# Optimization experiments

Hardware: AMD Instinct MI355X
Metric: run time of the kernel (lower is better)

The kernel has to match this reference:

```python
import jax, jax.numpy as jnp
import numpy as np

FEAT = 512
HEADS = 8
HEAD_DIM = FEAT // HEADS
HIDDEN = 2048
EPS = 1e-5


def _linear(x, W, b):
    # torch Linear: y = x @ W.T + b, W: (out, in)
    return jnp.einsum('bnd,od->bno', x, W) + b


def _layernorm(x, g, b):
    mu = jnp.mean(x, axis=-1, keepdims=True)
    var = jnp.var(x, axis=-1, keepdims=True)
    return (x - mu) * jax.lax.rsqrt(var + EPS) * g + b


def setup_inputs() -> dict:
    key = jax.random.key(0)
    ks = jax.random.split(key, 16)
    bsz, N = 16, 512
    gain = 2 ** (-0.5)
    lim = gain * np.sqrt(6.0 / (FEAT + FEAT))
    inp = {
        'nfeat': jax.random.normal(ks[0], (bsz, N, FEAT), jnp.float32),
        'attn_bias': jax.random.normal(ks[1], (bsz, N, N, HEADS), jnp.float32),
        'attn_mask': jax.random.randint(ks[2], (bsz, N, N), 0, 2, jnp.int32),
        'Wq': jax.random.uniform(ks[3], (FEAT, FEAT), jnp.float32, -lim, lim),
        'bq': jnp.zeros((FEAT,), jnp.float32),
        'Wk': jax.random.uniform(ks[4], (FEAT, FEAT), jnp.float32, -lim, lim),
        'bk': jnp.zeros((FEAT,), jnp.float32),
        'Wv': jax.random.uniform(ks[5], (FEAT, FEAT), jnp.float32, -lim, lim),
        'bv': jnp.zeros((FEAT,), jnp.float32),
        'Wo': jax.random.uniform(ks[6], (FEAT, FEAT), jnp.float32, -np.sqrt(6.0/(2*FEAT)), np.sqrt(6.0/(2*FEAT))),
        'bo': jnp.zeros((FEAT,), jnp.float32),
        'W1': jax.random.normal(ks[7], (HIDDEN, FEAT), jnp.float32) * 0.02,
        'b1': jnp.zeros((HIDDEN,), jnp.float32),
        'W2': jax.random.normal(ks[8], (FEAT, HIDDEN), jnp.float32) * 0.02,
        'b2': jnp.zeros((FEAT,), jnp.float32),
        'ln1_g': jnp.ones((FEAT,), jnp.float32),
        'ln1_b': jnp.zeros((FEAT,), jnp.float32),
        'ln2_g': jnp.ones((FEAT,), jnp.float32),
        'ln2_b': jnp.zeros((FEAT,), jnp.float32),
    }
    return inp


def reference(nfeat, attn_bias, attn_mask, Wq, bq, Wk, bk, Wv, bv, Wo, bo,
              W1, b1, W2, b2, ln1_g, ln1_b, ln2_g, ln2_b):
    bsz, N, _ = nfeat.shape
    residual = nfeat
    # --- biased multi-head attention (norm_first=False => no pre-norm) ---
    q = _linear(nfeat, Wq, bq).reshape(bsz, N, HEADS, HEAD_DIM)
    k = _linear(nfeat, Wk, bk).reshape(bsz, N, HEADS, HEAD_DIM)
    v = _linear(nfeat, Wv, bv).reshape(bsz, N, HEADS, HEAD_DIM)
    # NOTE: original code does q / scaling with scaling = head_dim**-0.5,
    # i.e. scores are MULTIPLIED by sqrt(head_dim) (faithful to source).
    scale = jnp.float32(HEAD_DIM ** 0.5)
    scores = jnp.einsum('bqhd,bkhd->bhqk', q, k) * scale  # (b,h,N,N)
    scores = scores + jnp.transpose(attn_bias, (0, 3, 1, 2))  # additive bias
    mask = (attn_mask != 0)[:, None, :, :]
    scores = jnp.where(mask, -jnp.inf, scores)
    attn = jax.nn.softmax(scores, axis=-1)
    ctx = jnp.einsum('bhqk,bkhd->bqhd', attn, v).reshape(bsz, N, FEAT)
    out = _linear(ctx, Wo, bo)
    x = residual + out
    x = _layernorm(x, ln1_g, ln1_b)
    # --- FFN ---
    residual = x
    h = jax.nn.relu(_linear(x, W1, b1))
    h = _linear(h, W2, b2)
    x = residual + h
    x = _layernorm(x, ln2_g, ln2_b)
    return x
```

## Files before the change

### kernel.cpp

```cpp
#include <hip/hip_runtime.h>
#include <hip/hip_bf16.h>
#include <stdint.h>

typedef unsigned short u16;
typedef __attribute__((ext_vector_type(8))) __bf16 bf16x8;
typedef __attribute__((ext_vector_type(4))) float f32x4;
typedef __attribute__((ext_vector_type(4))) unsigned short u16x4;

#define B_   16
#define N_   512
#define D_   512
#define H_   8
#define DH_  64
#define HID_ 2048
#define M_   8192

__device__ __forceinline__ u16 f2bf(float f) {
    unsigned u = __float_as_uint(f);
    u += 0x7fffu + ((u >> 16) & 1u);
    return (u16)(u >> 16);
}
__device__ __forceinline__ float bf2f(u16 u) {
    return __uint_as_float(((unsigned)u) << 16);
}
__device__ __forceinline__ f32x4 mfma16(bf16x8 a, bf16x8 b, f32x4 c) {
    return __builtin_amdgcn_mfma_f32_16x16x32_bf16(a, b, c, 0, 0, 0);
}
__device__ __forceinline__ void gload_lds16(const u16* g, u16* l) {
    __builtin_amdgcn_global_load_lds(
        (const __attribute__((address_space(1))) void*)g,
        (__attribute__((address_space(3))) void*)l, 16, 0, 0);
}

__device__ __forceinline__ void cvt4(const float* s, u16* d) {
    f32x4 v = *(const f32x4*)s;
    u16x4 o;
    o[0] = f2bf(v[0]); o[1] = f2bf(v[1]); o[2] = f2bf(v[2]); o[3] = f2bf(v[3]);
    *(u16x4*)d = o;
}
__device__ __forceinline__ void cvt4s(const float* s, u16* dh, u16* dl) {
    f32x4 v = *(const f32x4*)s;
    u16x4 oh, ol;
#pragma unroll
    for (int j = 0; j < 4; j++) {
        oh[j] = f2bf(v[j]);
        float r = v[j] - bf2f(oh[j]);
        ol[j] = f2bf(r);
    }
    *(u16x4*)dh = oh;
    *(u16x4*)dl = ol;
}

__global__ __launch_bounds__(256) void convert_all(
    const float* __restrict__ nf, const float* __restrict__ Wq,
    const float* __restrict__ Wk, const float* __restrict__ Wv,
    const float* __restrict__ Wo, const float* __restrict__ W1,
    const float* __restrict__ W2, const float* __restrict__ bq,
    const float* __restrict__ bk, const float* __restrict__ bv,
    u16* __restrict__ xh, u16* __restrict__ xl,
    u16* __restrict__ wqh, u16* __restrict__ wql,
    u16* __restrict__ wob, u16* __restrict__ w1b, u16* __restrict__ w2b,
    float* __restrict__ bqkv)
{
    long i = ((long)blockIdx.x * 256 + threadIdx.x) * 4;
    if (i < 4194304) { cvt4s(nf + i, xh + i, xl + i); return; }
    i -= 4194304;
    if (i < 786432) {
        const float* s = (i < 262144) ? (Wq + i)
                       : (i < 524288) ? (Wk + i - 262144) : (Wv + i - 524288);
        cvt4s(s, wqh + i, wql + i); return;
    }
    i -= 786432;
    if (i < 262144) { cvt4(Wo + i, wob + i); return; }
    i -= 262144;
    if (i < 1048576) { cvt4(W1 + i, w1b + i); return; }
    i -= 1048576;
    if (i < 1048576) { cvt4(W2 + i, w2b + i); return; }
    i -= 1048576;
    if (i < 1536) {
        const float* s = (i < 512) ? (bq + i) : (i < 1024 ? bk + i - 512 : bv + i - 1024);
        *(f32x4*)(bqkv + i) = *(const f32x4*)s;
    }
}

#define BM 128
#define BN 128
#define BK 32

__global__ __launch_bounds__(256) void gemm_qkv(
    const u16* __restrict__ Ah, const u16* __restrict__ Al,
    const u16* __restrict__ Wh, const u16* __restrict__ Wl,
    const float* __restrict__ bias,
    u16* __restrict__ Qh, u16* __restrict__ Ql,
    u16* __restrict__ Kh, u16* __restrict__ Kl, u16* __restrict__ Vt)
{
    __shared__ u16 sAh[BM * BK], sAl[BM * BK], sBh[BN * BK], sBl[BN * BK];
    const int Kdim = 512;
    const int tid = threadIdx.x;
    const int w = tid >> 6, lane = tid & 63;
    const int lr = lane & 15, lg = lane >> 4;
    const int nTn = 1536 / BN;
    const int tm = blockIdx.x / nTn, tn = blockIdx.x % nTn;
    const long m0 = (long)tm * BM, n0 = (long)tn * BN;
    const int which = (int)(n0 >> 9);
    const bool vpath = (which == 2);

    f32x4 acc[4][4];
#pragma unroll
    for (int i = 0; i < 4; i++)
#pragma unroll
        for (int j = 0; j < 4; j++) acc[i][j] = (f32x4){0.f, 0.f, 0.f, 0.f};

    const int e0 = w * 512 + lane * 8;
    const int r0 = e0 >> 5, c0 = e0 & 31;
    const int r1 = r0 + 64;
    const long gA0 = (long)r0 * Kdim + c0, gA1 = (long)r1 * Kdim + c0;
    const u16* pAh = Ah + m0 * Kdim;
    const u16* pAl = Al + m0 * Kdim;
    const u16* pBh = Wh + n0 * Kdim;
    const u16* pBl = Wl + n0 * Kdim;
    u16* dAh0 = sAh + w * 512; u16* dAh1 = sAh + w * 512 + 2048;
    u16* dAl0 = sAl + w * 512; u16* dAl1 = sAl + w * 512 + 2048;
    u16* dBh0 = sBh + w * 512; u16* dBh1 = sBh + w * 512 + 2048;
    u16* dBl0 = sBl + w * 512; u16* dBl1 = sBl + w * 512 + 2048;

    const int wr = (w >> 1) * 64, wc = (w & 1) * 64;

    for (int k0 = 0; k0 < Kdim; k0 += BK) {
        gload_lds16(pAh + gA0 + k0, dAh0);
        gload_lds16(pAh + gA1 + k0, dAh1);
        gload_lds16(pBh + gA0 + k0, dBh0);
        gload_lds16(pBh + gA1 + k0, dBh1);
        if (!vpath) {
            gload_lds16(pAl + gA0 + k0, dAl0);
            gload_lds16(pAl + gA1 + k0, dAl1);
            gload_lds16(pBl + gA0 + k0, dBl0);
            gload_lds16(pBl + gA1 + k0, dBl1);
        }
        __syncthreads();
        bf16x8 ah[4], bh[4];
#pragma unroll
        for (int i = 0; i < 4; i++) {
            int ra = (wr + i * 16 + lr) * BK + lg * 8;
            int rb = (wc + i * 16 + lr) * BK + lg * 8;
            ah[i] = *reinterpret_cast<const bf16x8*>(&sAh[ra]);
            bh[i] = *reinterpret_cast<const bf16x8*>(&sBh[rb]);
        }
        if (vpath) {
#pragma unroll
            for (int i = 0; i < 4; i++)
#pragma unroll
                for (int j = 0; j < 4; j++)
                    acc[i][j] = mfma16(ah[i], bh[j], acc[i][j]);
        } else {
            bf16x8 al[4], bl[4];
#pragma unroll
            for (int i = 0; i < 4; i++) {
                int ra = (wr + i * 16 + lr) * BK + lg * 8;
                int rb = (wc + i * 16 + lr) * BK + lg * 8;
                al[i] = *reinterpret_cast<const bf16x8*>(&sAl[ra]);
                bl[i] = *reinterpret_cast<const bf16x8*>(&sBl[rb]);
            }
#pragma unroll
            for (int i = 0; i < 4; i++)
#pragma unroll
                for (int j = 0; j < 4; j++) {
                    acc[i][j] = mfma16(ah[i], bh[j], acc[i][j]);
                    acc[i][j] = mfma16(ah[i], bl[j], acc[i][j]);
                    acc[i][j] = mfma16(al[i], bh[j], acc[i][j]);
                }
        }
        __syncthreads();
    }

#pragma unroll
    for (int i = 0; i < 4; i++) {
#pragma unroll
        for (int j = 0; j < 4; j++) {
#pragma unroll
            for (int r = 0; r < 4; r++) {
                long m = m0 + wr + i * 16 + lg * 4 + r;
                long n = n0 + wc + j * 16 + lr;
                float v = acc[i][j][r] + bias[n];
                int b = (int)(m >> 9), nn = (int)(m & 511);
                int h = ((int)n >> 6) & 7, dh = (int)n & 63;
                long bh_ = (long)b * 8 + h;
                if (which == 2) {
                    Vt[(bh_ * 64 + dh) * 512 + nn] = f2bf(v);
                } else {
                    u16 hi = f2bf(v);
                    u16 lo = f2bf(v - bf2f(hi));
                    long idx = (bh_ * 512 + nn) * 64 + dh;
                    if (which == 0) { Qh[idx] = hi; Ql[idx] = lo; }
                    else            { Kh[idx] = hi; Kl[idx] = lo; }
                }
            }
        }
    }
}

template<int EPI>
__global__ __launch_bounds__(256) void gemm_bt(
    const u16* __restrict__ A, const u16* __restrict__ W,
    const float* __restrict__ bias, const float* __restrict__ resid,
    float* __restrict__ outf, u16* __restrict__ outb,
    int Mdim, int Ndim, int Kdim)
{
    __shared__ u16 As[BM * BK];
    __shared__ u16 Bs[BN * BK];
    const int tid = threadIdx.x;
    const int w = tid >> 6, lane = tid & 63;
    const int lr = lane & 15, lg = lane >> 4;
    const int nTn = Ndim / BN;
    const int tm = blockIdx.x / nTn, tn = blockIdx.x % nTn;
    const long m0 = (long)tm * BM, n0 = (long)tn * BN;

    f32x4 acc[4][4];
#pragma unroll
    for (int i = 0; i < 4; i++)
#pragma unroll
        for (int j = 0; j < 4; j++) acc[i][j] = (f32x4){0.f, 0.f, 0.f, 0.f};

    const int e0 = w * 512 + lane * 8;
    const int r0 = e0 >> 5, c0 = e0 & 31;
    const int r1 = r0 + 64, c1 = c0;
    u16* As0 = As + w * 512;
    u16* As1 = As + w * 512 + 2048;
    u16* Bs0 = Bs + w * 512;
    u16* Bs1 = Bs + w * 512 + 2048;
    const u16* Ag = A + m0 * Kdim;
    const u16* Bg = W + n0 * Kdim;

    const int wr = (w >> 1) * 64, wc = (w & 1) * 64;

    for (int k0 = 0; k0 < Kdim; k0 += BK) {
        gload_lds16(Ag + (long)r0 * Kdim + k0 + c0, As0);
        gload_lds16(Ag + (long)r1 * Kdim + k0 + c1, As1);
        gload_lds16(Bg + (long)r0 * Kdim + k0 + c0, Bs0);
        gload_lds16(Bg + (long)r1 * Kdim + k0 + c1, Bs1);
        __syncthreads();
        bf16x8 af[4], bfr[4];
#pragma unroll
        for (int i = 0; i < 4; i++) {
            af[i]  = *reinterpret_cast<const bf16x8*>(&As[(wr + i * 16 + lr) * BK + lg * 8]);
            bfr[i] = *reinterpret_cast<const bf16x8*>(&Bs[(wc + i * 16 + lr) * BK + lg * 8]);
        }
#pragma unroll
        for (int i = 0; i < 4; i++)
#pragma unroll
            for (int j = 0; j < 4; j++)
                acc[i][j] = mfma16(af[i], bfr[j], acc[i][j]);
        __syncthreads();
    }

#pragma unroll
    for (int i = 0; i < 4; i++) {
#pragma unroll
        for (int j = 0; j < 4; j++) {
#pragma unroll
            for (int r = 0; r < 4; r++) {
                long m = m0 + wr + i * 16 + lg * 4 + r;
                long n = n0 + wc + j * 16 + lr;
                float v = acc[i][j][r];
                if (EPI == 1) {
                    long idx = m * Ndim + n;
                    outf[idx] = v + bias[n] + resid[idx];
                } else {
                    float t = v + bias[n];
                    t = t > 0.f ? t : 0.f;
                    outb[m * Ndim + n] = f2bf(t);
                }
            }
        }
    }
}

#define PLST 2116
#define PST  72

__global__ __launch_bounds__(512) void attn_kernel(
    const u16* __restrict__ Qh, const u16* __restrict__ Ql,
    const u16* __restrict__ Kh, const u16* __restrict__ Kl,
    const u16* __restrict__ Vt,
    const float* __restrict__ bias, const int* __restrict__ mask,
    u16* __restrict__ ctx)
{
    __shared__ float Bs[8 * PLST];
    __shared__ u16 Ps[8 * 32 * PST];
    const int tid = threadIdx.x;
    const int w = tid >> 6, lane = tid & 63;
    const int lr = lane & 15, lg = lane >> 4;
    const int b = blockIdx.x >> 4, qt = blockIdx.x & 15;
    const int bq0 = qt * 32;
    const long bh = (long)b * 8 + w;
    const u16* Qhp = Qh + bh * 512 * 64;
    const u16* Qlp = Ql + bh * 512 * 64;
    const u16* Khp = Kh + bh * 512 * 64;
    const u16* Klp = Kl + bh * 512 * 64;
    const u16* Vp  = Vt + bh * 64 * 512;

    const int sq = tid >> 4, st = tid & 15;
    const float* bias_row = bias + ((long)b * 512 + bq0 + sq) * 512 * 8;
    const int*   mask_row = mask + ((long)b * 512 + bq0 + sq) * 512;

    bf16x8 qhf[2][2], qlf[2][2];
#pragma unroll
    for (int mf = 0; mf < 2; mf++)
#pragma unroll
        for (int kk = 0; kk < 2; kk++) {
            long off = (long)(bq0 + mf * 16 + lr) * 64 + kk * 32 + lg * 8;
            qhf[mf][kk] = *reinterpret_cast<const bf16x8*>(&Qhp[off]);
            qlf[mf][kk] = *reinterpret_cast<const bf16x8*>(&Qlp[off]);
        }

    f32x4 of[2][4];
    float m_run[2][4], l_run[2][4];
#pragma unroll
    for (int mf = 0; mf < 2; mf++) {
#pragma unroll
        for (int df = 0; df < 4; df++) of[mf][df] = (f32x4){0.f, 0.f, 0.f, 0.f};
#pragma unroll
        for (int r = 0; r < 4; r++) { m_run[mf][r] = -1e30f; l_run[mf][r] = 0.f; }
    }

    float* Bw = Bs + w * PLST;
    u16* Pw = Ps + w * 32 * PST;

    for (int kt = 0; kt < 8; ++kt) {
        const int k0 = kt * 64;
        f32x4 breg[8];
        int mreg[8];
#pragma unroll
        for (int j = 0; j < 8; j++) {
            int f = st + j * 16;
            breg[j] = *(const f32x4*)(bias_row + (long)k0 * 8 + f * 4);
            mreg[j] = mask_row[k0 + (f >> 1)];
        }
        f32x4 s[2][4];
#pragma unroll
        for (int mf = 0; mf < 2; mf++)
#pragma unroll
            for (int kf = 0; kf < 4; kf++) s[mf][kf] = (f32x4){0.f, 0.f, 0.f, 0.f};
#pragma unroll
        for (int kf = 0; kf < 4; kf++) {
            long ko = (long)(k0 + kf * 16 + lr) * 64 + lg * 8;
            bf16x8 kh0 = *reinterpret_cast<const bf16x8*>(&Khp[ko]);
            bf16x8 kh1 = *reinterpret_cast<const bf16x8*>(&Khp[ko + 32]);
            bf16x8 kl0 = *reinterpret_cast<const bf16x8*>(&Klp[ko]);
            bf16x8 kl1 = *reinterpret_cast<const bf16x8*>(&Klp[ko + 32]);
#pragma unroll
            for (int mf = 0; mf < 2; mf++) {
                s[mf][kf] = mfma16(qhf[mf][0], kh0, s[mf][kf]);
                s[mf][kf] = mfma16(qhf[mf][1], kh1, s[mf][kf]);
                s[mf][kf] = mfma16(qhf[mf][0], kl0, s[mf][kf]);
                s[mf][kf] = mfma16(qhf[mf][1], kl1, s[mf][kf]);
                s[mf][kf] = mfma16(qlf[mf][0], kh0, s[mf][kf]);
                s[mf][kf] = mfma16(qlf[mf][1], kh1, s[mf][kf]);
            }
        }
        __syncthreads();
#pragma unroll
        for (int j = 0; j < 8; j++) {
            int f = st + j * 16;
            int k = f >> 1, h4 = (f & 1) * 4;
            bool msk = (mreg[j] != 0);
#pragma unroll
            for (int c = 0; c < 4; c++)
                Bs[(h4 + c) * PLST + sq * 66 + k] = msk ? -3e38f : breg[j][c];
        }
        __syncthreads();
#pragma unroll
        for (int mf = 0; mf < 2; mf++) {
#pragma unroll
            for (int r = 0; r < 4; r++) {
                int qrow = mf * 16 + lg * 4 + r;
#pragma unroll
                for (int kf = 0; kf < 4; kf++) {
                    int k = kf * 16 + lr;
                    s[mf][kf][r] = s[mf][kf][r] * 8.0f + Bw[qrow * 66 + k];
                }
            }
        }
#pragma unroll
        for (int mf = 0; mf < 2; mf++) {
#pragma unroll
            for (int r = 0; r < 4; r++) {
                float pm = s[mf][0][r];
#pragma unroll
                for (int kf = 1; kf < 4; kf++) pm = fmaxf(pm, s[mf][kf][r]);
                pm = fmaxf(pm, __shfl_xor(pm, 1));
                pm = fmaxf(pm, __shfl_xor(pm, 2));
                pm = fmaxf(pm, __shfl_xor(pm, 4));
                pm = fmaxf(pm, __shfl_xor(pm, 8));
                float mn = fmaxf(m_run[mf][r], pm);
                float fac = __expf(m_run[mf][r] - mn);
                m_run[mf][r] = mn;
                float rs = 0.f;
#pragma unroll
                for (int kf = 0; kf < 4; kf++) {
                    float p = __expf(s[mf][kf][r] - mn);
                    s[mf][kf][r] = p;
                    rs += p;
                }
                rs += __shfl_xor(rs, 1); rs += __shfl_xor(rs, 2);
                rs += __shfl_xor(rs, 4); rs += __shfl_xor(rs, 8);
                l_run[mf][r] = l_run[mf][r] * fac + rs;
#pragma unroll
                for (int df = 0; df < 4; df++) of[mf][df][r] *= fac;
            }
        }
#pragma unroll
        for (int mf = 0; mf < 2; mf++)
#pragma unroll
            for (int kf = 0; kf < 4; kf++)
#pragma unroll
                for (int r = 0; r < 4; r++)
                    Pw[(mf * 16 + lg * 4 + r) * PST + kf * 16 + lr] = f2bf(s[mf][kf][r]);
#pragma unroll
        for (int kk = 0; kk < 2; kk++) {
            bf16x8 pa[2];
#pragma unroll
            for (int mf = 0; mf < 2; mf++)
                pa[mf] = *reinterpret_cast<const bf16x8*>(
                    &Pw[(mf * 16 + lr) * PST + kk * 32 + lg * 8]);
#pragma unroll
            for (int df = 0; df < 4; df++) {
                bf16x8 vb = *reinterpret_cast<const bf16x8*>(
                    &Vp[(long)(df * 16 + lr) * 512 + k0 + kk * 32 + lg * 8]);
                of[0][df] = mfma16(pa[0], vb, of[0][df]);
                of[1][df] = mfma16(pa[1], vb, of[1][df]);
            }
        }
    }
#pragma unroll
    for (int mf = 0; mf < 2; mf++) {
#pragma unroll
        for (int r = 0; r < 4; r++) {
            int q = bq0 + mf * 16 + lg * 4 + r;
            float inv = 1.0f / l_run[mf][r];
            u16* crow = ctx + ((long)b * 512 + q) * 512 + w * 64;
#pragma unroll
            for (int df = 0; df < 4; df++)
                crow[df * 16 + lr] = f2bf(of[mf][df][r] * inv);
        }
    }
}

template<int WB>
__global__ __launch_bounds__(256) void ln_kernel(
    const float* __restrict__ xin, const float* __restrict__ g,
    const float* __restrict__ bta, float* __restrict__ fout, u16* __restrict__ bout)
{
    const int tid = threadIdx.x;
    const int w = tid >> 6, lane = tid & 63;
    const long row = (long)blockIdx.x * 4 + w;
    const float* xp = xin + row * 512 + lane * 8;
    f32x4 v0 = *(const f32x4*)(xp);
    f32x4 v1 = *(const f32x4*)(xp + 4);
    float sum = v0[0] + v0[1] + v0[2] + v0[3] + v1[0] + v1[1] + v1[2] + v1[3];
    float sq = v0[0]*v0[0] + v0[1]*v0[1] + v0[2]*v0[2] + v0[3]*v0[3]
             + v1[0]*v1[0] + v1[1]*v1[1] + v1[2]*v1[2] + v1[3]*v1[3];
#pragma unroll
    for (int m = 1; m <= 32; m <<= 1) {
        sum += __shfl_xor(sum, m);
        sq  += __shfl_xor(sq, m);
    }
    float mu = sum * (1.f / 512.f);
    float var = sq * (1.f / 512.f) - mu * mu;
    float rstd = rsqrtf(var + 1e-5f);
#pragma unroll
    for (int j = 0; j < 8; j++) {
        int c = lane * 8 + j;
        float x = (j < 4) ? v0[j] : v1[j - 4];
        float y = (x - mu) * rstd * g[c] + bta[c];
        fout[row * 512 + c] = y;
        if (WB) bout[row * 512 + c] = f2bf(y);
    }
}

extern "C" void kernel_launch(void* const* d_in, const int* in_sizes, int n_in,
                              void* d_out, int out_size, void* d_ws, size_t ws_size,
                              hipStream_t stream)
{
    const float* nfeat     = (const float*)d_in[0];
    const float* attn_bias = (const float*)d_in[1];
    const int*   attn_mask = (const int*)d_in[2];
    const float* Wq = (const float*)d_in[3];
    const float* bq = (const float*)d_in[4];
    const float* Wk = (const float*)d_in[5];
    const float* bk = (const float*)d_in[6];
    const float* Wv = (const float*)d_in[7];
    const float* bv = (const float*)d_in[8];
    const float* Wo = (const float*)d_in[9];
    const float* bo = (const float*)d_in[10];
    const float* W1 = (const float*)d_in[11];
    const float* b1 = (const float*)d_in[12];
    const float* W2 = (const float*)d_in[13];
    const float* b2 = (const float*)d_in[14];
    const float* ln1_g = (const float*)d_in[15];
    const float* ln1_b = (const float*)d_in[16];
    const float* ln2_g = (const float*)d_in[17];
    const float* ln2_b = (const float*)d_in[18];

    char* ws = (char*)d_ws;
    size_t off = 0;
    auto alloc = [&](size_t bytes) -> void* {
        void* p = ws + off;
        off += (bytes + 255) & ~(size_t)255;
        return p;
    };
    u16* xh    = (u16*)alloc((size_t)M_ * D_ * 2);
    u16* xl    = (u16*)alloc((size_t)M_ * D_ * 2);
    u16* wqh   = (u16*)alloc((size_t)1536 * 512 * 2);
    u16* wql   = (u16*)alloc((size_t)1536 * 512 * 2);
    u16* wob   = (u16*)alloc((size_t)512 * 512 * 2);
    u16* w1b   = (u16*)alloc((size_t)2048 * 512 * 2);
    u16* w2b   = (u16*)alloc((size_t)512 * 2048 * 2);
    float* bqkv = (float*)alloc(1536 * 4);
    u16* Qh    = (u16*)alloc((size_t)B_ * H_ * N_ * DH_ * 2);
    u16* Ql    = (u16*)alloc((size_t)B_ * H_ * N_ * DH_ * 2);
    u16* Kh    = (u16*)alloc((size_t)B_ * H_ * N_ * DH_ * 2);
    u16* Kl    = (u16*)alloc((size_t)B_ * H_ * N_ * DH_ * 2);
    u16* Vt    = (u16*)alloc((size_t)B_ * H_ * N_ * DH_ * 2);
    u16* ctx   = (u16*)alloc((size_t)M_ * D_ * 2);
    float* xres = (float*)alloc((size_t)M_ * D_ * 4);
    float* x1f  = (float*)alloc((size_t)M_ * D_ * 4);
    u16* x1b   = (u16*)alloc((size_t)M_ * D_ * 2);
    u16* hb    = (u16*)alloc((size_t)M_ * HID_ * 2);

    convert_all<<<7170, 256, 0, stream>>>(nfeat, Wq, Wk, Wv, Wo, W1, W2, bq, bk, bv,
                                          xh, xl, wqh, wql, wob, w1b, w2b, bqkv);
    gemm_qkv<<<(M_/BM) * (1536/BN), 256, 0, stream>>>(
        xh, xl, wqh, wql, bqkv, Qh, Ql, Kh, Kl, Vt);
    attn_kernel<<<B_ * 16, 512, 0, stream>>>(
        Qh, Ql, Kh, Kl, Vt, attn_bias, attn_mask, ctx);
    gemm_bt<1><<<(M_/BM) * (512/BN), 256, 0, stream>>>(
        ctx, wob, bo, nfeat, xres, nullptr, M_, 512, 512);
    ln_kernel<1><<<M_ / 4, 256, 0, stream>>>(xres, ln1_g, ln1_b, x1f, x1b);
    gemm_bt<2><<<(M_/BM) * (HID_/BN), 256, 0, stream>>>(
        x1b, w1b, b1, nullptr, nullptr, hb, M_, HID_, 512);
    gemm_bt<1><<<(M_/BM) * (512/BN), 256, 0, stream>>>(
        hb, w2b, b2, x1f, xres, nullptr, M_, 512, 2048);
    ln_kernel<0><<<M_ / 4, 256, 0, stream>>>(xres, ln2_g, ln2_b, (float*)d_out, nullptr);
}
```

Baseline: 516.5 us.

## Store Q/K/V in MFMA fragment layout and halve attention query tile with bias prefetch

The QKV GEMM epilogue now writes Q, K and V directly in a per-lane MFMA fragment order, so each attention lane reads its operand with one contiguous 16-byte load instead of strided row reads. The attention kernel drops from 32 to 16 query rows per block, doubling the grid to 512 blocks to raise occupancy and parallelism. It double-buffers the bias and mask register loads so the next tile's fetch is issued while the current tile computes, and it raises wave priority around the MFMA sequences. The cost is that K and V fragments are re-read twice as often across blocks, and the epilogue now writes scattered addresses.

```diff
diff --git a/kernel.cpp b/kernel.cpp
--- a/kernel.cpp
+++ b/kernel.cpp
@@ -14,6 +14,7 @@
 #define DH_  64
 #define HID_ 2048
 #define M_   8192
+#define FRAG_BH 32768
 
 __device__ __forceinline__ u16 f2bf(float f) {
     unsigned u = __float_as_uint(f);
@@ -91,8 +92,8 @@
     const u16* __restrict__ Ah, const u16* __restrict__ Al,
     const u16* __restrict__ Wh, const u16* __restrict__ Wl,
     const float* __restrict__ bias,
-    u16* __restrict__ Qh, u16* __restrict__ Ql,
-    u16* __restrict__ Kh, u16* __restrict__ Kl, u16* __restrict__ Vt)
+    u16* __restrict__ Qf, u16* __restrict__ Qlf,
+    u16* __restrict__ Kf, u16* __restrict__ Klf, u16* __restrict__ Vf)
 {
     __shared__ u16 sAh[BM * BK], sAl[BM * BK], sBh[BN * BK], sBl[BN * BK];
     const int Kdim = 512;
@@ -186,13 +187,18 @@
                 int h = ((int)n >> 6) & 7, dh = (int)n & 63;
                 long bh_ = (long)b * 8 + h;
                 if (which == 2) {
-                    Vt[(bh_ * 64 + dh) * 512 + nn] = f2bf(v);
+                    int df = dh >> 4, rho = dh & 15;
+                    int gam = (nn >> 3) & 3, e = nn & 7, nb32 = nn >> 5;
+                    Vf[bh_ * FRAG_BH + (((long)nb32 * 4 + df) * 64 + gam * 16 + rho) * 8 + e]
+                        = f2bf(v);
                 } else {
+                    int nb = nn >> 4, rho = nn & 15;
+                    int kk = dh >> 5, gam = (dh >> 3) & 3, e = dh & 7;
+                    long idx = bh_ * FRAG_BH + (((long)nb * 2 + kk) * 64 + gam * 16 + rho) * 8 + e;
                     u16 hi = f2bf(v);
                     u16 lo = f2bf(v - bf2f(hi));
-                    long idx = (bh_ * 512 + nn) * 64 + dh;
-                    if (which == 0) { Qh[idx] = hi; Ql[idx] = lo; }
-                    else            { Kh[idx] = hi; Kl[idx] = lo; }
+                    if (which == 0) { Qf[idx] = hi; Qlf[idx] = lo; }
+                    else            { Kf[idx] = hi; Klf[idx] = lo; }
                 }
             }
         }
@@ -275,174 +281,162 @@
     }
 }
 
-#define PLST 2116
+#define PLST 1060
 #define PST  72
 
 __global__ __launch_bounds__(512) void attn_kernel(
-    const u16* __restrict__ Qh, const u16* __restrict__ Ql,
-    const u16* __restrict__ Kh, const u16* __restrict__ Kl,
-    const u16* __restrict__ Vt,
+    const u16* __restrict__ Qf, const u16* __restrict__ Qlf,
+    const u16* __restrict__ Kf, const u16* __restrict__ Klf,
+    const u16* __restrict__ Vf,
     const float* __restrict__ bias, const int* __restrict__ mask,
     u16* __restrict__ ctx)
 {
     __shared__ float Bs[8 * PLST];
-    __shared__ u16 Ps[8 * 32 * PST];
+    __shared__ u16 Ps[8 * 16 * PST];
     const int tid = threadIdx.x;
     const int w = tid >> 6, lane = tid & 63;
     const int lr = lane & 15, lg = lane >> 4;
-    const int b = blockIdx.x >> 4, qt = blockIdx.x & 15;
-    const int bq0 = qt * 32;
+    const int b = blockIdx.x >> 5, qt = blockIdx.x & 31;
+    const int bq0 = qt * 16;
     const long bh = (long)b * 8 + w;
-    const u16* Qhp = Qh + bh * 512 * 64;
-    const u16* Qlp = Ql + bh * 512 * 64;
-    const u16* Khp = Kh + bh * 512 * 64;
-    const u16* Klp = Kl + bh * 512 * 64;
-    const u16* Vp  = Vt + bh * 64 * 512;
-
-    const int sq = tid >> 4, st = tid & 15;
+    const u16* Qfp  = Qf  + bh * FRAG_BH;
+    const u16* Qlfp = Qlf + bh * FRAG_BH;
+    const u16* Kfp  = Kf  + bh * FRAG_BH;
+    const u16* Klfp = Klf + bh * FRAG_BH;
+    const u16* Vfp  = Vf  + bh * FRAG_BH;
+
+    const int sq = tid >> 5, st = tid & 31;
     const float* bias_row = bias + ((long)b * 512 + bq0 + sq) * 512 * 8;
     const int*   mask_row = mask + ((long)b * 512 + bq0 + sq) * 512;
 
-    bf16x8 qhf[2][2], qlf[2][2];
-#pragma unroll
-    for (int mf = 0; mf < 2; mf++)
+    bf16x8 qhf[2], qlf[2];
+#pragma unroll
+    for (int kk = 0; kk < 2; kk++) {
+        long off = (((long)qt * 2 + kk) * 64 + lane) * 8;
+        qhf[kk] = *reinterpret_cast<const bf16x8*>(&Qfp[off]);
+        qlf[kk] = *reinterpret_cast<const bf16x8*>(&Qlfp[off]);
+    }
+
+    f32x4 of[4];
+    float m_run[4], l_run[4];
+#pragma unroll
+    for (int df = 0; df < 4; df++) of[df] = (f32x4){0.f, 0.f, 0.f, 0.f};
+#pragma unroll
+    for (int r = 0; r < 4; r++) { m_run[r] = -1e30f; l_run[r] = 0.f; }
+
+    float* Bw = Bs + w * PLST;
+    u16* Pw = Ps + w * 16 * PST;
+
+    f32x4 bA[4], bB[4];
+    int mA[4], mB[4];
+
+    auto loadbias = [&](int kt, f32x4 (&bb)[4], int (&mm)[4]) {
+#pragma unroll
+        for (int j = 0; j < 4; j++) {
+            int f = st + j * 32;
+            bb[j] = *(const f32x4*)(bias_row + (long)kt * 512 + f * 4);
+            mm[j] = mask_row[kt * 64 + (f >> 1)];
+        }
+    };
+
+    auto body = [&](int kt, f32x4 (&bc)[4], int (&mc)[4],
+                    f32x4 (&bn)[4], int (&mn)[4], bool pf) {
+        f32x4 s[4];
+#pragma unroll
+        for (int kf = 0; kf < 4; kf++) s[kf] = (f32x4){0.f, 0.f, 0.f, 0.f};
+#pragma unroll
+        for (int kf = 0; kf < 4; kf++) {
+            long kb = (((long)(kt * 4 + kf) * 2) * 64 + lane) * 8;
+            bf16x8 kh0 = *reinterpret_cast<const bf16x8*>(&Kfp[kb]);
+            bf16x8 kh1 = *reinterpret_cast<const bf16x8*>(&Kfp[kb + 512]);
+            bf16x8 kl0 = *reinterpret_cast<const bf16x8*>(&Klfp[kb]);
+            bf16x8 kl1 = *reinterpret_cast<const bf16x8*>(&Klfp[kb + 512]);
+            __builtin_amdgcn_s_setprio(1);
+            s[kf] = mfma16(qhf[0], kh0, s[kf]);
+            s[kf] = mfma16(qhf[1], kh1, s[kf]);
+            s[kf] = mfma16(qhf[0], kl0, s[kf]);
+            s[kf] = mfma16(qhf[1], kl1, s[kf]);
+            s[kf] = mfma16(qlf[0], kh0, s[kf]);
+            s[kf] = mfma16(qlf[1], kh1, s[kf]);
+            __builtin_amdgcn_s_setprio(0);
+        }
+        __syncthreads();
+#pragma unroll
+        for (int j = 0; j < 4; j++) {
+            int f = st + j * 32;
+            int k = f >> 1, h4 = (f & 1) * 4;
+            bool msk = (mc[j] != 0);
+#pragma unroll
+            for (int c = 0; c < 4; c++)
+                Bs[(h4 + c) * PLST + sq * 66 + k] = msk ? -3e38f : bc[j][c];
+        }
+        __syncthreads();
+        if (pf) loadbias(kt + 1, bn, mn);
+#pragma unroll
+        for (int r = 0; r < 4; r++) {
+            int qrow = lg * 4 + r;
+#pragma unroll
+            for (int kf = 0; kf < 4; kf++)
+                s[kf][r] = s[kf][r] * 8.0f + Bw[qrow * 66 + kf * 16 + lr];
+        }
+#pragma unroll
+        for (int r = 0; r < 4; r++) {
+            float pm = fmaxf(fmaxf(s[0][r], s[1][r]), fmaxf(s[2][r], s[3][r]));
+            pm = fmaxf(pm, __shfl_xor(pm, 1));
+            pm = fmaxf(pm, __shfl_xor(pm, 2));
+            pm = fmaxf(pm, __shfl_xor(pm, 4));
+            pm = fmaxf(pm, __shfl_xor(pm, 8));
+            float mn_ = fmaxf(m_run[r], pm);
+            float fac = __expf(m_run[r] - mn_);
+            m_run[r] = mn_;
+            float rs = 0.f;
+#pragma unroll
+            for (int kf = 0; kf < 4; kf++) {
+                float p = __expf(s[kf][r] - mn_);
+                s[kf][r] = p;
+                rs += p;
+            }
+            rs += __shfl_xor(rs, 1); rs += __shfl_xor(rs, 2);
+            rs += __shfl_xor(rs, 4); rs += __shfl_xor(rs, 8);
+            l_run[r] = l_run[r] * fac + rs;
+#pragma unroll
+            for (int df = 0; df < 4; df++) of[df][r] *= fac;
+        }
+#pragma unroll
+        for (int kf = 0; kf < 4; kf++)
+#pragma unroll
+            for (int r = 0; r < 4; r++)
+                Pw[(lg * 4 + r) * PST + kf * 16 + lr] = f2bf(s[kf][r]);
 #pragma unroll
         for (int kk = 0; kk < 2; kk++) {
-            long off = (long)(bq0 + mf * 16 + lr) * 64 + kk * 32 + lg * 8;
-            qhf[mf][kk] = *reinterpret_cast<const bf16x8*>(&Qhp[off]);
-            qlf[mf][kk] = *reinterpret_cast<const bf16x8*>(&Qlp[off]);
-        }
-
-    f32x4 of[2][4];
-    float m_run[2][4], l_run[2][4];
-#pragma unroll
-    for (int mf = 0; mf < 2; mf++) {
-#pragma unroll
-        for (int df = 0; df < 4; df++) of[mf][df] = (f32x4){0.f, 0.f, 0.f, 0.f};
-#pragma unroll
-        for (int r = 0; r < 4; r++) { m_run[mf][r] = -1e30f; l_run[mf][r] = 0.f; }
-    }
-
-    float* Bw = Bs + w * PLST;
-    u16* Pw = Ps + w * 32 * PST;
-
-    for (int kt = 0; kt < 8; ++kt) {
-        const int k0 = kt * 64;
-        f32x4 breg[8];
-        int mreg[8];
-#pragma unroll
-        for (int j = 0; j < 8; j++) {
-            int f = st + j * 16;
-            breg[j] = *(const f32x4*)(bias_row + (long)k0 * 8 + f * 4);
-            mreg[j] = mask_row[k0 + (f >> 1)];
-        }
-        f32x4 s[2][4];
-#pragma unroll
-        for (int mf = 0; mf < 2; mf++)
-#pragma unroll
-            for (int kf = 0; kf < 4; kf++) s[mf][kf] = (f32x4){0.f, 0.f, 0.f, 0.f};
-#pragma unroll
-        for (int kf = 0; kf < 4; kf++) {
-            long ko = (long)(k0 + kf * 16 + lr) * 64 + lg * 8;
-            bf16x8 kh0 = *reinterpret_cast<const bf16x8*>(&Khp[ko]);
-            bf16x8 kh1 = *reinterpret_cast<const bf16x8*>(&Khp[ko + 32]);
-            bf16x8 kl0 = *reinterpret_cast<const bf16x8*>(&Klp[ko]);
-            bf16x8 kl1 = *reinterpret_cast<const bf16x8*>(&Klp[ko + 32]);
-#pragma unroll
-            for (int mf = 0; mf < 2; mf++) {
-                s[mf][kf] = mfma16(qhf[mf][0], kh0, s[mf][kf]);
-                s[mf][kf] = mfma16(qhf[mf][1], kh1, s[mf][kf]);
-                s[mf][kf] = mfma16(qhf[mf][0], kl0, s[mf][kf]);
-                s[mf][kf] = mfma16(qhf[mf][1], kl1, s[mf][kf]);
-                s[mf][kf] = mfma16(qlf[mf][0], kh0, s[mf][kf]);
-                s[mf][kf] = mfma16(qlf[mf][1], kh1, s[mf][kf]);
-            }
-        }
-        __syncthreads();
-#pragma unroll
-        for (int j = 0; j < 8; j++) {
-            int f = st + j * 16;
-            int k = f >> 1, h4 = (f & 1) * 4;
-            bool msk = (mreg[j] != 0);
-#pragma unroll
-            for (int c = 0; c < 4; c++)
-                Bs[(h4 + c) * PLST + sq * 66 + k] = msk ? -3e38f : breg[j][c];
-        }
-        __syncthreads();
-#pragma unroll
-        for (int mf = 0; mf < 2; mf++) {
-#pragma unroll
-            for (int r = 0; r < 4; r++) {
-                int qrow = mf * 16 + lg * 4 + r;
-#pragma unroll
-                for (int kf = 0; kf < 4; kf++) {
-                    int k = kf * 16 + lr;
-                    s[mf][kf][r] = s[mf][kf][r] * 8.0f + Bw[qrow * 66 + k];
-                }
-            }
-        }
-#pragma unroll
-        for (int mf = 0; mf < 2; mf++) {
-#pragma unroll
-            for (int r = 0; r < 4; r++) {
-                float pm = s[mf][0][r];
-#pragma unroll
-                for (int kf = 1; kf < 4; kf++) pm = fmaxf(pm, s[mf][kf][r]);
-                pm = fmaxf(pm, __shfl_xor(pm, 1));
-                pm = fmaxf(pm, __shfl_xor(pm, 2));
-                pm = fmaxf(pm, __shfl_xor(pm, 4));
-                pm = fmaxf(pm, __shfl_xor(pm, 8));
-                float mn = fmaxf(m_run[mf][r], pm);
-                float fac = __expf(m_run[mf][r] - mn);
-                m_run[mf][r] = mn;
-                float rs = 0.f;
-#pragma unroll
-                for (int kf = 0; kf < 4; kf++) {
-                    float p = __expf(s[mf][kf][r] - mn);
-                    s[mf][kf][r] = p;
-                    rs += p;
-                }
-                rs += __shfl_xor(rs, 1); rs += __shfl_xor(rs, 2);
-                rs += __shfl_xor(rs, 4); rs += __shfl_xor(rs, 8);
-                l_run[mf][r] = l_run[mf][r] * fac + rs;
-#pragma unroll
-                for (int df = 0; df < 4; df++) of[mf][df][r] *= fac;
-            }
-        }
-#pragma unroll
-        for (int mf = 0; mf < 2; mf++)
-#pragma unroll
-            for (int kf = 0; kf < 4; kf++)
-#pragma unroll
-                for (int r = 0; r < 4; r++)
-                    Pw[(mf * 16 + lg * 4 + r) * PST + kf * 16 + lr] = f2bf(s[mf][kf][r]);
-#pragma unroll
-        for (int kk = 0; kk < 2; kk++) {
-            bf16x8 pa[2];
-#pragma unroll
-            for (int mf = 0; mf < 2; mf++)
-                pa[mf] = *reinterpret_cast<const bf16x8*>(
-                    &Pw[(mf * 16 + lr) * PST + kk * 32 + lg * 8]);
+            bf16x8 pa = *reinterpret_cast<const bf16x8*>(
+                &Pw[lr * PST + kk * 32 + lg * 8]);
 #pragma unroll
             for (int df = 0; df < 4; df++) {
                 bf16x8 vb = *reinterpret_cast<const bf16x8*>(
-                    &Vp[(long)(df * 16 + lr) * 512 + k0 + kk * 32 + lg * 8]);
-                of[0][df] = mfma16(pa[0], vb, of[0][df]);
-                of[1][df] = mfma16(pa[1], vb, of[1][df]);
+                    &Vfp[((((long)(kt * 2 + kk)) * 4 + df) * 64 + lane) * 8]);
+                __builtin_amdgcn_s_setprio(1);
+                of[df] = mfma16(pa, vb, of[df]);
+                __builtin_amdgcn_s_setprio(0);
             }
         }
-    }
-#pragma unroll
-    for (int mf = 0; mf < 2; mf++) {
-#pragma unroll
-        for (int r = 0; r < 4; r++) {
-            int q = bq0 + mf * 16 + lg * 4 + r;
-            float inv = 1.0f / l_run[mf][r];
-            u16* crow = ctx + ((long)b * 512 + q) * 512 + w * 64;
-#pragma unroll
-            for (int df = 0; df < 4; df++)
-                crow[df * 16 + lr] = f2bf(of[mf][df][r] * inv);
-        }
+    };
+
+    loadbias(0, bA, mA);
+#pragma unroll
+    for (int kt2 = 0; kt2 < 4; kt2++) {
+        body(kt2 * 2,     bA, mA, bB, mB, true);
+        body(kt2 * 2 + 1, bB, mB, bA, mA, kt2 < 3);
+    }
+
+#pragma unroll
+    for (int r = 0; r < 4; r++) {
+        int q = bq0 + lg * 4 + r;
+        float inv = 1.0f / l_run[r];
+        u16* crow = ctx + ((long)b * 512 + q) * 512 + w * 64;
+#pragma unroll
+        for (int df = 0; df < 4; df++)
+            crow[df * 16 + lr] = f2bf(of[df][r] * inv);
     }
 }
 
@@ -517,11 +511,11 @@
     u16* w1b   = (u16*)alloc((size_t)2048 * 512 * 2);
     u16* w2b   = (u16*)alloc((size_t)512 * 2048 * 2);
     float* bqkv = (float*)alloc(1536 * 4);
-    u16* Qh    = (u16*)alloc((size_t)B_ * H_ * N_ * DH_ * 2);
-    u16* Ql    = (u16*)alloc((size_t)B_ * H_ * N_ * DH_ * 2);
-    u16* Kh    = (u16*)alloc((size_t)B_ * H_ * N_ * DH_ * 2);
-    u16* Kl    = (u16*)alloc((size_t)B_ * H_ * N_ * DH_ * 2);
-    u16* Vt    = (u16*)alloc((size_t)B_ * H_ * N_ * DH_ * 2);
+    u16* Qf    = (u16*)alloc((size_t)128 * FRAG_BH * 2);
+    u16* Qlf   = (u16*)alloc((size_t)128 * FRAG_BH * 2);
+    u16* Kf    = (u16*)alloc((size_t)128 * FRAG_BH * 2);
+    u16* Klf   = (u16*)alloc((size_t)128 * FRAG_BH * 2);
+    u16* Vf    = (u16*)alloc((size_t)128 * FRAG_BH * 2);
     u16* ctx   = (u16*)alloc((size_t)M_ * D_ * 2);
     float* xres = (float*)alloc((size_t)M_ * D_ * 4);
     float* x1f  = (float*)alloc((size_t)M_ * D_ * 4);
@@ -531,9 +525,9 @@
     convert_all<<<7170, 256, 0, stream>>>(nfeat, Wq, Wk, Wv, Wo, W1, W2, bq, bk, bv,
                                           xh, xl, wqh, wql, wob, w1b, w2b, bqkv);
     gemm_qkv<<<(M_/BM) * (1536/BN), 256, 0, stream>>>(
-        xh, xl, wqh, wql, bqkv, Qh, Ql, Kh, Kl, Vt);
-    attn_kernel<<<B_ * 16, 512, 0, stream>>>(
-        Qh, Ql, Kh, Kl, Vt, attn_bias, attn_mask, ctx);
+        xh, xl, wqh, wql, bqkv, Qf, Qlf, Kf, Klf, Vf);
+    attn_kernel<<<B_ * 32, 512, 0, stream>>>(
+        Qf, Qlf, Kf, Klf, Vf, attn_bias, attn_mask, ctx);
     gemm_bt<1><<<(M_/BM) * (512/BN), 256, 0, stream>>>(
         ctx, wob, bo, nfeat, xres, nullptr, M_, 512, 512);
     ln_kernel<1><<<M_ / 4, 256, 0, stream>>>(xres, ln1_g, ln1_b, x1f, x1b);
```

Result: faster. 504.2 us (-2.4%).
